# Kernel optimization log

Hardware: AMD Instinct MI355X
Metric: run time of the kernel (lower is better)

## Reference

```python
import jax, jax.numpy as jnp
import numpy as np

B, D, T, K = 16, 512, 4096, 1024
COMMIT = 0.25


def setup_inputs() -> dict:
    key = jax.random.key(0)
    kx, ke = jax.random.split(key)
    x = jax.random.normal(kx, (B, D, T), dtype=jnp.float32)
    # nn.init.uniform_(weight, -1/K, 1/K)
    embedding = jax.random.uniform(ke, (K, D), dtype=jnp.float32,
                                   minval=-1.0 / K, maxval=1.0 / K)
    return {"x": x, "embedding": embedding}


def reference(x, embedding):
    # x: [B, D, T] -> [B, T, D]
    xt = jnp.transpose(x, (0, 2, 1))
    xf = xt.reshape(-1, xt.shape[-1])  # [N, D], N = B*T
    dist = (jnp.sum(xf * xf, axis=1, keepdims=True)
            + jnp.sum(embedding * embedding, axis=1)
            - 2.0 * (xf @ embedding.T))
    idx = jnp.argmin(dist, axis=1)  # [N]
    # one-hot @ embedding == gather
    quantized = jnp.take(embedding, idx, axis=0).reshape(xt.shape)  # [B, T, D]
    commitment_loss = COMMIT * jnp.mean((jax.lax.stop_gradient(quantized) - xt) ** 2)
    embedding_loss = jnp.mean((quantized - jax.lax.stop_gradient(xt)) ** 2)
    loss = commitment_loss + embedding_loss
    # straight-through estimator
    quantized_st = xt + jax.lax.stop_gradient(quantized - xt)
    encoding_indices = idx.reshape(xt.shape[0], xt.shape[1], 1)
    return quantized_st, loss, encoding_indices
```

## Files before the change

kernel.cpp:

```cpp
#include <hip/hip_runtime.h>

#define BB 16
#define DD 512
#define TT 4096
#define KK 1024
#define NN (BB*TT)
#define RWS 32
#define BT 512
#define NW 8
#define MARGIN 1e-3f
#define CM 6
#define PM 192
#define XLD 516
#define NPART (NN/RWS)

typedef __attribute__((ext_vector_type(8))) short short8v;
typedef __attribute__((ext_vector_type(4))) float f32x4;

__device__ __forceinline__ unsigned short f2bf(float f) {
    unsigned int u = __float_as_uint(f);
    unsigned int r = (u + 0x7fffu + ((u >> 16) & 1u)) >> 16;
    return (unsigned short)r;
}

__device__ __forceinline__ float pw128_sq_strided(const float* a, int stride) {
    float V[16];
    #pragma unroll
    for (int l = 0; l < 16; ++l) {
        float q[8];
        #pragma unroll
        for (int k = 0; k < 8; ++k) {
            float e = a[(l + 16 * k) * stride];
            q[k] = __fmul_rn(e, e);
        }
        V[l] = __fadd_rn(__fadd_rn(__fadd_rn(q[0], q[1]), __fadd_rn(q[2], q[3])),
                         __fadd_rn(__fadd_rn(q[4], q[5]), __fadd_rn(q[6], q[7])));
    }
    float u[8];
    #pragma unroll
    for (int l = 0; l < 8; ++l) u[l] = __fadd_rn(V[l], V[l + 8]);
    float v[4];
    #pragma unroll
    for (int l = 0; l < 4; ++l) v[l] = __fadd_rn(u[l], u[l + 4]);
    return __fadd_rn(__fadd_rn(v[0], v[2]), __fadd_rn(v[1], v[3]));
}
__device__ __forceinline__ float pw512_sq_strided(const float* a, int stride) {
    float p0 = pw128_sq_strided(a, stride);
    float p1 = pw128_sq_strided(a + 128 * stride, stride);
    float p2 = pw128_sq_strided(a + 256 * stride, stride);
    float p3 = pw128_sq_strided(a + 384 * stride, stride);
    return __fadd_rn(__fadd_rn(p0, p1), __fadd_rn(p2, p3));
}

__global__ void enorms_exact(const float* __restrict__ E, float* __restrict__ se) {
    int i = blockIdx.x * blockDim.x + threadIdx.x;
    if (i < KK) se[i] = pw512_sq_strided(E + (long)i * DD, 1);
}

__global__ void pack_e(const float* __restrict__ E, unsigned short* __restrict__ Bph) {
    int i = blockIdx.x * blockDim.x + threadIdx.x;
    if (i >= KK * DD / 2) return;
    int c = i >> 8;
    int k = (i & 255) * 2;
    float2 v = *reinterpret_cast<const float2*>(E + ((long)c << 9) + k);
    int lane = (c & 15) + ((k >> 3) & 3) * 16;
    int hw = (((c >> 4) * 16 + (k >> 5)) * 64 + lane) * 8 + (k & 7);
    unsigned int pk = (unsigned int)f2bf(v.x) | ((unsigned int)f2bf(v.y) << 16);
    *reinterpret_cast<unsigned int*>(Bph + hw) = pk;
}

__device__ __forceinline__ short8v build_frag_rm(const float* __restrict__ row, int c0) {
    union { short8v v; unsigned int wd[4]; } u;
    float4 a = *reinterpret_cast<const float4*>(row + c0);
    float4 b = *reinterpret_cast<const float4*>(row + c0 + 4);
    asm("v_cvt_pk_bf16_f32 %0, %1, %2" : "=v"(u.wd[0]) : "v"(a.x), "v"(a.y));
    asm("v_cvt_pk_bf16_f32 %0, %1, %2" : "=v"(u.wd[1]) : "v"(a.z), "v"(a.w));
    asm("v_cvt_pk_bf16_f32 %0, %1, %2" : "=v"(u.wd[2]) : "v"(b.x), "v"(b.y));
    asm("v_cvt_pk_bf16_f32 %0, %1, %2" : "=v"(u.wd[3]) : "v"(b.z), "v"(b.w));
    return u.v;
}

__global__ __launch_bounds__(BT)
void vq_fused(const float* __restrict__ x, const float* __restrict__ E,
              const unsigned short* __restrict__ Bph,
              const float* __restrict__ se,
              double* __restrict__ partials, float* __restrict__ out) {
    __shared__ __align__(16) float xsf[RWS * XLD];
    __shared__ float wrowmin[NW * RWS];
    __shared__ float gthr[RWS];
    __shared__ int   rcnt[RWS];
    __shared__ unsigned short rc[RWS][CM];
    __shared__ int   prow[PM];
    __shared__ int   pcand[PM];
    __shared__ unsigned long long rmin[RWS];
    __shared__ float sxs[RWS];
    __shared__ int   fidx[RWS];
    __shared__ int   oflag[RWS];
    __shared__ double wloss[NW];
    __shared__ int   pcnt, oany;

    const int tid  = threadIdx.x;
    const int w    = tid >> 6;
    const int lane = tid & 63;
    const int blk  = blockIdx.x;
    const int b    = blk >> 7;
    const int t0   = (blk & 127) * RWS;
    const long nbase = (long)b * TT + t0;
    const float* xb = x + (long)b * DD * TT + t0;

    if (tid < RWS) { rcnt[tid] = 0; rmin[tid] = ~0ull; oflag[tid] = 0; fidx[tid] = -1; }
    if (tid == 0) { pcnt = 0; oany = 0; }

    {
        const int r  = lane & 31;
        const int dh = lane >> 5;
        const float* xbl = xb + r;
        #pragma unroll
        for (int it = 0; it < 4; ++it) {
            int d0 = ((it * NW + w) * 2 + dh) * 8;
            float v[8];
            #pragma unroll
            for (int jj = 0; jj < 8; ++jj)
                v[jj] = xbl[(long)(d0 + jj) * TT];
            float4 lo = {v[0], v[1], v[2], v[3]};
            float4 hi = {v[4], v[5], v[6], v[7]};
            *reinterpret_cast<float4*>(&xsf[r * XLD + d0])     = lo;
            *reinterpret_cast<float4*>(&xsf[r * XLD + d0 + 4]) = hi;
        }
    }
    __syncthreads();

    f32x4 acc[2][8];
    #pragma unroll
    for (int m = 0; m < 2; ++m)
        #pragma unroll
        for (int n = 0; n < 8; ++n)
            acc[m][n] = (f32x4){0.f, 0.f, 0.f, 0.f};

    const short8v* Bhv = (const short8v*)Bph;
    {
        const int rl  = lane & 15;
        const int lg8 = (lane >> 4) * 8;
        for (int kk = 0; kk < 16; ++kk) {
            short8v ah[2];
            #pragma unroll
            for (int m = 0; m < 2; ++m)
                ah[m] = build_frag_rm(xsf + (m * 16 + rl) * XLD, kk * 32 + lg8);
            #pragma unroll
            for (int nh = 0; nh < 2; ++nh) {
                short8v bh[4];
                #pragma unroll
                for (int q = 0; q < 4; ++q)
                    bh[q] = Bhv[((w * 8 + nh * 4 + q) * 16 + kk) * 64 + lane];
                #pragma unroll
                for (int q = 0; q < 4; ++q)
                    #pragma unroll
                    for (int m = 0; m < 2; ++m)
                        acc[m][nh * 4 + q] = __builtin_amdgcn_mfma_f32_16x16x32_bf16(
                            ah[m], bh[q], acc[m][nh * 4 + q], 0, 0, 0);
            }
        }
    }

    float sef[8];
    #pragma unroll
    for (int n = 0; n < 8; ++n) sef[n] = se[w * 128 + n * 16 + (lane & 15)];

    #pragma unroll
    for (int m = 0; m < 2; ++m) {
        #pragma unroll
        for (int r4 = 0; r4 < 4; ++r4) {
            float mn = 1e30f;
            #pragma unroll
            for (int n = 0; n < 8; ++n)
                mn = fminf(mn, fmaf(-2.f, acc[m][n][r4], sef[n]));
            #pragma unroll
            for (int off = 1; off < 16; off <<= 1)
                mn = fminf(mn, __shfl_xor(mn, off, 64));
            if ((lane & 15) == 0)
                wrowmin[w * RWS + m * 16 + (lane >> 4) * 4 + r4] = mn;
        }
    }
    __syncthreads();

    if (tid < RWS) {
        float g = 1e30f;
        #pragma unroll
        for (int ww = 0; ww < NW; ++ww)
            g = fminf(g, wrowmin[ww * RWS + tid]);
        gthr[tid] = g + MARGIN;
    }
    __syncthreads();

    #pragma unroll
    for (int m = 0; m < 2; ++m) {
        #pragma unroll
        for (int r4 = 0; r4 < 4; ++r4) {
            int row = m * 16 + (lane >> 4) * 4 + r4;
            float th = gthr[row];
            #pragma unroll
            for (int n = 0; n < 8; ++n) {
                float sc = fmaf(-2.f, acc[m][n][r4], sef[n]);
                if (sc <= th) {
                    int pos = atomicAdd(&rcnt[row], 1);
                    if (pos < CM)
                        rc[row][pos] = (unsigned short)(w * 128 + n * 16 + (lane & 15));
                }
            }
        }
    }
    {
        int r = tid >> 4, l = tid & 15;
        const float* bp = xsf + r * XLD;
        float pblk[4];
        #pragma unroll
        for (int kb = 0; kb < 4; ++kb) {
            float q[8];
            #pragma unroll
            for (int k = 0; k < 8; ++k) {
                float e = bp[kb * 128 + l + 16 * k];
                q[k] = __fmul_rn(e, e);
            }
            float V = __fadd_rn(__fadd_rn(__fadd_rn(q[0], q[1]), __fadd_rn(q[2], q[3])),
                                __fadd_rn(__fadd_rn(q[4], q[5]), __fadd_rn(q[6], q[7])));
            V = __fadd_rn(V, __shfl_xor(V, 8, 16));
            V = __fadd_rn(V, __shfl_xor(V, 4, 16));
            V = __fadd_rn(V, __shfl_xor(V, 2, 16));
            V = __fadd_rn(V, __shfl_xor(V, 1, 16));
            pblk[kb] = V;
        }
        if (l == 0)
            sxs[r] = __fadd_rn(__fadd_rn(pblk[0], pblk[1]), __fadd_rn(pblk[2], pblk[3]));
    }
    __syncthreads();

    if (tid < RWS) {
        int cnt = rcnt[tid];
        if (cnt == 1) {
            fidx[tid] = (int)rc[tid][0];
        } else if (cnt <= CM) {
            int base = atomicAdd(&pcnt, cnt);
            for (int i = 0; i < cnt; ++i) {
                prow[base + i]  = tid;
                pcand[base + i] = (int)rc[tid][i];
            }
        } else {
            oflag[tid] = 1;
            atomicOr(&oany, 1);
        }
    }
    __syncthreads();

    const int np = (pcnt < PM) ? pcnt : PM;
    {
        int p = lane * NW + w;
        if (p < np) {
            int r = prow[p], c = pcand[p];
            const float4* Ep4 = reinterpret_cast<const float4*>(E + (long)c * DD);
            const float4* Xp4 = reinterpret_cast<const float4*>(xsf + r * XLD);
            float g = 0.f;
            #pragma unroll 4
            for (int jj = 0; jj < 128; ++jj) {
                float4 e4 = Ep4[jj], x4 = Xp4[jj];
                g = __fmaf_rn(x4.x, e4.x, g);
                g = __fmaf_rn(x4.y, e4.y, g);
                g = __fmaf_rn(x4.z, e4.z, g);
                g = __fmaf_rn(x4.w, e4.w, g);
            }
            float t1 = __fadd_rn(sxs[r], se[c]);
            float d  = __fsub_rn(t1, __fmul_rn(2.f, g));
            unsigned int bb = __float_as_uint(d);
            unsigned int u  = (bb & 0x80000000u) ? ~bb : (bb | 0x80000000u);
            atomicMin(&rmin[r], ((unsigned long long)u << 10) | (unsigned int)c);
        }
    }
    __syncthreads();

    if (tid < RWS && fidx[tid] < 0 && !oflag[tid])
        fidx[tid] = (int)(rmin[tid] & 0x3ffu);

    if (oany) {
        for (int r = 0; r < RWS; ++r) {
            if (!oflag[r]) continue;
            const float4* Xp4 = reinterpret_cast<const float4*>(xsf + r * XLD);
            float bd = 1e30f; int bi = KK;
            #pragma unroll
            for (int q = 0; q < 2; ++q) {
                int c = q * BT + tid;
                const float4* Ep4 = reinterpret_cast<const float4*>(E + (long)c * DD);
                float g = 0.f;
                #pragma unroll 4
                for (int jj = 0; jj < 128; ++jj) {
                    float4 e4 = Ep4[jj], x4 = Xp4[jj];
                    g = __fmaf_rn(x4.x, e4.x, g);
                    g = __fmaf_rn(x4.y, e4.y, g);
                    g = __fmaf_rn(x4.z, e4.z, g);
                    g = __fmaf_rn(x4.w, e4.w, g);
                }
                float d = __fsub_rn(__fadd_rn(sxs[r], se[c]), __fmul_rn(2.f, g));
                if (d < bd) { bd = d; bi = c; }
            }
            #pragma unroll
            for (int off = 32; off; off >>= 1) {
                float tv = __shfl_down(bd, off, 64);
                int   ti = __shfl_down(bi, off, 64);
                if (tv < bd || (tv == bd && ti < bi)) { bd = tv; bi = ti; }
            }
            if (lane == 0) {
                unsigned int bb = __float_as_uint(bd);
                unsigned int u  = (bb & 0x80000000u) ? ~bb : (bb | 0x80000000u);
                atomicMin(&rmin[r], ((unsigned long long)u << 10) | (unsigned int)bi);
            }
            __syncthreads();
            if (tid == 0) fidx[r] = (int)(rmin[r] & 0x3ffu);
        }
    }
    __syncthreads();

    if (tid < RWS)
        out[(size_t)NN * DD + 1 + nbase + tid] = (float)fidx[tid];

    double lacc = 0.0;
    #pragma unroll
    for (int it = 0; it < 8; ++it) {
        int flat = it * BT + tid;
        int r = flat >> 7;
        int j = (flat & 127) * 4;
        int idx = fidx[r];
        float4 ev = *reinterpret_cast<const float4*>(E + (long)idx * DD + j);
        float4 xv = *reinterpret_cast<const float4*>(&xsf[r * XLD + j]);
        float d0 = __fsub_rn(ev.x, xv.x);
        float d1 = __fsub_rn(ev.y, xv.y);
        float d2 = __fsub_rn(ev.z, xv.z);
        float d3 = __fsub_rn(ev.w, xv.w);
        float4 st;
        st.x = __fadd_rn(xv.x, d0); st.y = __fadd_rn(xv.y, d1);
        st.z = __fadd_rn(xv.z, d2); st.w = __fadd_rn(xv.w, d3);
        *reinterpret_cast<float4*>(out + (size_t)(nbase + r) * DD + j) = st;
        lacc += (double)d0 * d0 + (double)d1 * d1 + (double)d2 * d2 + (double)d3 * d3;
    }
    #pragma unroll
    for (int off = 32; off; off >>= 1) lacc += __shfl_down(lacc, off, 64);
    if (lane == 0) wloss[w] = lacc;
    __syncthreads();
    if (tid == 0) {
        double s = 0.0;
        #pragma unroll
        for (int ww = 0; ww < NW; ++ww) s += wloss[ww];
        partials[blk] = s;
    }
}

__global__ void finalize_kernel(const double* __restrict__ partials, float* __restrict__ out) {
    __shared__ double sm[16];
    const int tid = threadIdx.x;
    const int w = tid >> 6, lane = tid & 63;
    double a = partials[tid] + partials[tid + 1024];
    #pragma unroll
    for (int off = 32; off; off >>= 1) a += __shfl_down(a, off, 64);
    if (lane == 0) sm[w] = a;
    __syncthreads();
    if (tid == 0) {
        double s = 0.0;
        #pragma unroll
        for (int i = 0; i < 16; ++i) s += sm[i];
        out[(size_t)NN * DD] = (float)(1.25 * s / ((double)NN * DD));
    }
}

extern "C" void kernel_launch(void* const* d_in, const int* in_sizes, int n_in,
                              void* d_out, int out_size, void* d_ws, size_t ws_size,
                              hipStream_t stream) {
    const float* x = (const float*)d_in[0];
    const float* E = (const float*)d_in[1];
    float* out = (float*)d_out;
    double* partials = (double*)d_ws;
    float* se = (float*)((char*)d_ws + 32768);
    unsigned short* Bph = (unsigned short*)((char*)d_ws + 65536);

    enorms_exact<<<4, 256, 0, stream>>>(E, se);
    pack_e<<<(KK * DD / 2) / 256, 256, 0, stream>>>(E, Bph);
    vq_fused<<<NPART, BT, 0, stream>>>(x, E, Bph, se, partials, out);
    finalize_kernel<<<1, 1024, 0, stream>>>(partials, out);
}
```

Baseline: 224.5 us.

## Cut block barriers in VQ argmin via atomic row minima and static candidate slots

Replaces the per-wave row-minimum array and its separate reduction with a shared atomicMin on order-preserving float keys, moves the x-norm computation ahead of that barrier, and gives candidate refinement fixed (row, slot) positions instead of building a compacted list. Together these remove two or three __syncthreads phases. The global x load becomes float4 reads along T with scalar transposed LDS writes, and the MFMA loop is wrapped with s_setprio. The scalar LDS stores may cause bank conflicts, and the fixed slots leave more lanes idle during refinement.

```diff
diff --git a/kernel.cpp b/kernel.cpp
--- a/kernel.cpp
+++ b/kernel.cpp
@@ -10,7 +10,6 @@
 #define NW 8
 #define MARGIN 1e-3f
 #define CM 6
-#define PM 192
 #define XLD 516
 #define NPART (NN/RWS)
 
@@ -21,6 +20,15 @@
     unsigned int u = __float_as_uint(f);
     unsigned int r = (u + 0x7fffu + ((u >> 16) & 1u)) >> 16;
     return (unsigned short)r;
+}
+
+__device__ __forceinline__ unsigned int f2sort(float f) {
+    unsigned int b = __float_as_uint(f);
+    return (b & 0x80000000u) ? ~b : (b | 0x80000000u);
+}
+__device__ __forceinline__ float sort2f(unsigned int u) {
+    unsigned int b = (u & 0x80000000u) ? (u & 0x7fffffffu) : ~u;
+    return __uint_as_float(b);
 }
 
 __device__ __forceinline__ float pw128_sq_strided(const float* a, int stride) {
@@ -86,18 +94,15 @@
               const float* __restrict__ se,
               double* __restrict__ partials, float* __restrict__ out) {
     __shared__ __align__(16) float xsf[RWS * XLD];
-    __shared__ float wrowmin[NW * RWS];
-    __shared__ float gthr[RWS];
+    __shared__ unsigned int rowmin[RWS];
     __shared__ int   rcnt[RWS];
     __shared__ unsigned short rc[RWS][CM];
-    __shared__ int   prow[PM];
-    __shared__ int   pcand[PM];
     __shared__ unsigned long long rmin[RWS];
     __shared__ float sxs[RWS];
     __shared__ int   fidx[RWS];
     __shared__ int   oflag[RWS];
     __shared__ double wloss[NW];
-    __shared__ int   pcnt, oany;
+    __shared__ int   oany;
 
     const int tid  = threadIdx.x;
     const int w    = tid >> 6;
@@ -108,24 +113,23 @@
     const long nbase = (long)b * TT + t0;
     const float* xb = x + (long)b * DD * TT + t0;
 
-    if (tid < RWS) { rcnt[tid] = 0; rmin[tid] = ~0ull; oflag[tid] = 0; fidx[tid] = -1; }
-    if (tid == 0) { pcnt = 0; oany = 0; }
+    if (tid < RWS) {
+        rcnt[tid] = 0; rowmin[tid] = 0xFFFFFFFFu; rmin[tid] = ~0ull;
+        oflag[tid] = 0; fidx[tid] = -1;
+    }
+    if (tid == 0) oany = 0;
 
     {
-        const int r  = lane & 31;
-        const int dh = lane >> 5;
-        const float* xbl = xb + r;
-        #pragma unroll
-        for (int it = 0; it < 4; ++it) {
-            int d0 = ((it * NW + w) * 2 + dh) * 8;
-            float v[8];
-            #pragma unroll
-            for (int jj = 0; jj < 8; ++jj)
-                v[jj] = xbl[(long)(d0 + jj) * TT];
-            float4 lo = {v[0], v[1], v[2], v[3]};
-            float4 hi = {v[4], v[5], v[6], v[7]};
-            *reinterpret_cast<float4*>(&xsf[r * XLD + d0])     = lo;
-            *reinterpret_cast<float4*>(&xsf[r * XLD + d0 + 4]) = hi;
+        const int t4  = (lane & 7) * 4;
+        const int dof = lane >> 3;
+        #pragma unroll
+        for (int it = 0; it < 8; ++it) {
+            int d = (it * NW + w) * 8 + dof;
+            float4 v = *reinterpret_cast<const float4*>(xb + (long)d * TT + t4);
+            xsf[(t4 + 0) * XLD + d] = v.x;
+            xsf[(t4 + 1) * XLD + d] = v.y;
+            xsf[(t4 + 2) * XLD + d] = v.z;
+            xsf[(t4 + 3) * XLD + d] = v.w;
         }
     }
     __syncthreads();
@@ -152,12 +156,14 @@
                 #pragma unroll
                 for (int q = 0; q < 4; ++q)
                     bh[q] = Bhv[((w * 8 + nh * 4 + q) * 16 + kk) * 64 + lane];
+                __builtin_amdgcn_s_setprio(1);
                 #pragma unroll
                 for (int q = 0; q < 4; ++q)
                     #pragma unroll
                     for (int m = 0; m < 2; ++m)
                         acc[m][nh * 4 + q] = __builtin_amdgcn_mfma_f32_16x16x32_bf16(
                             ah[m], bh[q], acc[m][nh * 4 + q], 0, 0, 0);
+                __builtin_amdgcn_s_setprio(0);
             }
         }
     }
@@ -178,17 +184,31 @@
             for (int off = 1; off < 16; off <<= 1)
                 mn = fminf(mn, __shfl_xor(mn, off, 64));
             if ((lane & 15) == 0)
-                wrowmin[w * RWS + m * 16 + (lane >> 4) * 4 + r4] = mn;
-        }
-    }
-    __syncthreads();
-
-    if (tid < RWS) {
-        float g = 1e30f;
-        #pragma unroll
-        for (int ww = 0; ww < NW; ++ww)
-            g = fminf(g, wrowmin[ww * RWS + tid]);
-        gthr[tid] = g + MARGIN;
+                atomicMin(&rowmin[m * 16 + (lane >> 4) * 4 + r4], f2sort(mn));
+        }
+    }
+    {
+        int r = tid >> 4, l = tid & 15;
+        const float* bp = xsf + r * XLD;
+        float pblk[4];
+        #pragma unroll
+        for (int kb = 0; kb < 4; ++kb) {
+            float q[8];
+            #pragma unroll
+            for (int k = 0; k < 8; ++k) {
+                float e = bp[kb * 128 + l + 16 * k];
+                q[k] = __fmul_rn(e, e);
+            }
+            float V = __fadd_rn(__fadd_rn(__fadd_rn(q[0], q[1]), __fadd_rn(q[2], q[3])),
+                                __fadd_rn(__fadd_rn(q[4], q[5]), __fadd_rn(q[6], q[7])));
+            V = __fadd_rn(V, __shfl_xor(V, 8, 16));
+            V = __fadd_rn(V, __shfl_xor(V, 4, 16));
+            V = __fadd_rn(V, __shfl_xor(V, 2, 16));
+            V = __fadd_rn(V, __shfl_xor(V, 1, 16));
+            pblk[kb] = V;
+        }
+        if (l == 0)
+            sxs[r] = __fadd_rn(__fadd_rn(pblk[0], pblk[1]), __fadd_rn(pblk[2], pblk[3]));
     }
     __syncthreads();
 
@@ -197,7 +217,7 @@
         #pragma unroll
         for (int r4 = 0; r4 < 4; ++r4) {
             int row = m * 16 + (lane >> 4) * 4 + r4;
-            float th = gthr[row];
+            float th = sort2f(rowmin[row]) + MARGIN;
             #pragma unroll
             for (int n = 0; n < 8; ++n) {
                 float sc = fmaf(-2.f, acc[m][n][r4], sef[n]);
@@ -209,53 +229,14 @@
             }
         }
     }
-    {
-        int r = tid >> 4, l = tid & 15;
-        const float* bp = xsf + r * XLD;
-        float pblk[4];
-        #pragma unroll
-        for (int kb = 0; kb < 4; ++kb) {
-            float q[8];
-            #pragma unroll
-            for (int k = 0; k < 8; ++k) {
-                float e = bp[kb * 128 + l + 16 * k];
-                q[k] = __fmul_rn(e, e);
-            }
-            float V = __fadd_rn(__fadd_rn(__fadd_rn(q[0], q[1]), __fadd_rn(q[2], q[3])),
-                                __fadd_rn(__fadd_rn(q[4], q[5]), __fadd_rn(q[6], q[7])));
-            V = __fadd_rn(V, __shfl_xor(V, 8, 16));
-            V = __fadd_rn(V, __shfl_xor(V, 4, 16));
-            V = __fadd_rn(V, __shfl_xor(V, 2, 16));
-            V = __fadd_rn(V, __shfl_xor(V, 1, 16));
-            pblk[kb] = V;
-        }
-        if (l == 0)
-            sxs[r] = __fadd_rn(__fadd_rn(pblk[0], pblk[1]), __fadd_rn(pblk[2], pblk[3]));
-    }
-    __syncthreads();
-
-    if (tid < RWS) {
-        int cnt = rcnt[tid];
-        if (cnt == 1) {
-            fidx[tid] = (int)rc[tid][0];
-        } else if (cnt <= CM) {
-            int base = atomicAdd(&pcnt, cnt);
-            for (int i = 0; i < cnt; ++i) {
-                prow[base + i]  = tid;
-                pcand[base + i] = (int)rc[tid][i];
-            }
-        } else {
-            oflag[tid] = 1;
-            atomicOr(&oany, 1);
-        }
-    }
-    __syncthreads();
-
-    const int np = (pcnt < PM) ? pcnt : PM;
-    {
-        int p = lane * NW + w;
-        if (p < np) {
-            int r = prow[p], c = pcand[p];
+    __syncthreads();
+
+    if (lane < 24) {
+        int s = lane * 8 + w;
+        int r = s / CM, ci = s - r * CM;
+        int cnt = rcnt[r];
+        if (cnt >= 2 && cnt <= CM && ci < cnt) {
+            int c = (int)rc[r][ci];
             const float4* Ep4 = reinterpret_cast<const float4*>(E + (long)c * DD);
             const float4* Xp4 = reinterpret_cast<const float4*>(xsf + r * XLD);
             float g = 0.f;
@@ -269,15 +250,19 @@
             }
             float t1 = __fadd_rn(sxs[r], se[c]);
             float d  = __fsub_rn(t1, __fmul_rn(2.f, g));
-            unsigned int bb = __float_as_uint(d);
-            unsigned int u  = (bb & 0x80000000u) ? ~bb : (bb | 0x80000000u);
-            atomicMin(&rmin[r], ((unsigned long long)u << 10) | (unsigned int)c);
-        }
-    }
-    __syncthreads();
-
-    if (tid < RWS && fidx[tid] < 0 && !oflag[tid])
-        fidx[tid] = (int)(rmin[tid] & 0x3ffu);
+            unsigned long long key = ((unsigned long long)f2sort(d) << 10) | (unsigned int)c;
+            atomicMin(&rmin[r], key);
+        }
+    }
+    __syncthreads();
+
+    if (tid < RWS) {
+        int cnt = rcnt[tid];
+        if (cnt == 1)                   fidx[tid] = (int)rc[tid][0];
+        else if (cnt >= 2 && cnt <= CM) fidx[tid] = (int)(rmin[tid] & 0x3ffu);
+        else { oflag[tid] = 1; atomicOr(&oany, 1); }
+    }
+    __syncthreads();
 
     if (oany) {
         for (int r = 0; r < RWS; ++r) {
@@ -307,12 +292,12 @@
                 if (tv < bd || (tv == bd && ti < bi)) { bd = tv; bi = ti; }
             }
             if (lane == 0) {
-                unsigned int bb = __float_as_uint(bd);
-                unsigned int u  = (bb & 0x80000000u) ? ~bb : (bb | 0x80000000u);
-                atomicMin(&rmin[r], ((unsigned long long)u << 10) | (unsigned int)bi);
+                unsigned long long key = ((unsigned long long)f2sort(bd) << 10) | (unsigned int)bi;
+                atomicMin(&rmin[r], key);
             }
             __syncthreads();
             if (tid == 0) fidx[r] = (int)(rmin[r] & 0x3ffu);
+            __syncthreads();
         }
     }
     __syncthreads();
```

Result: faster. 211.8 us (-5.7%).
